# Optimization experiments

Measured on AMD Instinct MI355X. Metric: run time of the kernel, lower is better.

Reference implementation:

```python
import jax, jax.numpy as jnp
import numpy as np

BN_EPS = 1e-5
BIND_CHAN = 4  # hparams.MODEL.LEARNABLE_OFFSET.BIND_CHAN


def conv1x1(x, w, b):
    # x: [B,C,H,W], w: [O,C], b: [O]
    return jnp.einsum('bchw,oc->bohw', x, w) + b[None, :, None, None]


def bn_train(x, gamma, beta):
    # training-mode batch norm over (B,H,W) per channel
    mean = jnp.mean(x, axis=(0, 2, 3), keepdims=True)
    var = jnp.var(x, axis=(0, 2, 3), keepdims=True)
    xn = (x - mean) * jax.lax.rsqrt(var + BN_EPS)
    return xn * gamma[None, :, None, None] + beta[None, :, None, None]


def displace_channel(x, offsets):
    # x: [B,C,H,W]; offsets: [C,2] (dy,dx) per channel, continuous.
    # out[b,c,y,x] = bilinear sample of x[b,c] at (y+dy_c, x+dx_c), zeros outside.
    B, C, H, W = x.shape
    dy, dx = offsets[:, 0], offsets[:, 1]
    fy, fx = jnp.floor(dy), jnp.floor(dx)
    wy, wx = dy - fy, dx - fx          # fractional weights, [C]
    iy, ix = fy.astype(jnp.int32), fx.astype(jnp.int32)
    chan = jnp.arange(C)[:, None, None]

    def shifted(oy, ox):
        ys = jnp.arange(H)[None, :] + oy[:, None]   # [C,H]
        xs = jnp.arange(W)[None, :] + ox[:, None]   # [C,W]
        valid = ((ys >= 0) & (ys < H))[:, :, None] & ((xs >= 0) & (xs < W))[:, None, :]
        ysc = jnp.clip(ys, 0, H - 1)
        xsc = jnp.clip(xs, 0, W - 1)
        g = x[:, chan, ysc[:, :, None], xsc[:, None, :]]   # [B,C,H,W]
        return g * valid.astype(x.dtype)[None]

    w00 = ((1 - wy) * (1 - wx))[None, :, None, None]
    w01 = ((1 - wy) * wx)[None, :, None, None]
    w10 = (wy * (1 - wx))[None, :, None, None]
    w11 = (wy * wx)[None, :, None, None]
    return (w00 * shifted(iy, ix) + w01 * shifted(iy, ix + 1)
            + w10 * shifted(iy + 1, ix) + w11 * shifted(iy + 1, ix + 1))


def setup_inputs() -> dict:
    key = jax.random.key(0)
    ks = jax.random.split(key, 12)
    B, Cin, H, W = 16, 64, 128, 128
    Cd, Cout = 128, 64
    n_off = Cd // BIND_CHAN  # 32
    s_in = 1.0 / np.sqrt(Cin)
    s_d = 1.0 / np.sqrt(Cd)
    return {
        'x': jax.random.normal(ks[0], (B, Cin, H, W), jnp.float32),
        'pre_w': jax.random.uniform(ks[1], (Cd, Cin), jnp.float32, -s_in, s_in),
        'pre_b': jax.random.uniform(ks[2], (Cd,), jnp.float32, -s_in, s_in),
        'post_w': jax.random.uniform(ks[3], (Cout, Cd), jnp.float32, -s_d, s_d),
        'post_b': jax.random.uniform(ks[4], (Cout,), jnp.float32, -s_d, s_d),
        'atten_w': jax.random.uniform(ks[5], (Cd, Cin), jnp.float32, -s_in, s_in),
        'atten_b': jax.random.uniform(ks[6], (Cd,), jnp.float32, -s_in, s_in),
        'atten_bn_g': jnp.ones((Cd,), jnp.float32),
        'atten_bn_b': jnp.zeros((Cd,), jnp.float32),
        'offsets': jax.random.normal(ks[7], (n_off, 2), jnp.float32) * 3.0,
        'bn_g': jnp.ones((Cout,), jnp.float32),
        'bn_b': jnp.zeros((Cout,), jnp.float32),
    }


def reference(x, pre_w, pre_b, post_w, post_b, atten_w, atten_b,
              atten_bn_g, atten_bn_b, offsets, bn_g, bn_b):
    # pre_offset conv1x1
    out_pre = conv1x1(x, pre_w, pre_b)                        # [B,Cd,H,W]
    # DisplaceChannel: each offset shared by BIND_CHAN consecutive channels
    off_per_chan = jnp.repeat(offsets, BIND_CHAN, axis=0)     # [Cd,2]
    out_dis = displace_channel(out_pre, off_per_chan)
    # Attention branch: conv1x1 -> BN -> Softplus -> SpaceNormalization
    a = conv1x1(x, atten_w, atten_b)
    a = bn_train(a, atten_bn_g, atten_bn_b)
    a = jax.nn.softplus(a)
    out_atten = a / jnp.sum(a, axis=(2, 3), keepdims=True)    # spatial normalization
    # post_offset conv1x1 on gated displaced features
    out_post = conv1x1(out_atten * out_dis, post_w, post_b)
    # residual (inplanes == outplanes, stride 1 -> no downsample) + BN + ReLU
    out_skip = x + out_post
    return jax.nn.relu(bn_train(out_skip, bn_g, bn_b))
```

## Files before the change

### kernel.cpp

```cpp
#include <hip/hip_runtime.h>

#define HWSZ   16384
#define CIN    64
#define CD     128
#define COUT   64
#define BN_EPS 1e-5f

typedef __attribute__((ext_vector_type(8))) short short8x;
typedef __attribute__((ext_vector_type(4))) float floatx4;

#define WS_WT1   0
#define WS_WTP   16384
#define WS_DISP  24576
#define WS_ASTAT 25344
#define WS_OSTAT 25600
#define WS_BIG   32768
#define WS_TOTAL_BYTES ((size_t)(32768 + 16777216) * 4)

__device__ __forceinline__ unsigned short f2bf(float f) {
    unsigned int u = __float_as_uint(f);
    u += 0x7fff + ((u >> 16) & 1);
    return (unsigned short)(u >> 16);
}
__device__ __forceinline__ float bf2f(unsigned short s) {
    return __uint_as_float(((unsigned int)s) << 16);
}
__device__ __forceinline__ float softplus_fast(float x) {
    return fmaxf(x, 0.f) + __logf(1.f + __expf(-fabsf(x)));
}
__device__ __forceinline__ float block_reduce(float v, float* sc) {
    #pragma unroll
    for (int off = 32; off >= 1; off >>= 1) v += __shfl_xor(v, off, 64);
    int wv = threadIdx.x >> 6, ln = threadIdx.x & 63;
    int nw = blockDim.x >> 6;
    if (ln == 0) sc[wv] = v;
    __syncthreads();
    float r = ((int)threadIdx.x < nw) ? sc[threadIdx.x] : 0.f;
    r += __shfl_xor(r, 1, 64);
    r += __shfl_xor(r, 2, 64);
    r += __shfl_xor(r, 4, 64);
    return r;
}

__global__ __launch_bounds__(256) void prep_kernel(
        const float* __restrict__ pre_w, const float* __restrict__ atten_w,
        const float* __restrict__ post_w, const float* __restrict__ offsets,
        float* __restrict__ ws) {
    int tid = blockIdx.x * 256 + threadIdx.x;
    unsigned short* wAB = (unsigned short*)(ws + WS_WT1);
    unsigned short* wP  = (unsigned short*)(ws + WS_WTP);
    float* disp = ws + WS_DISP;
    if (tid < 16384) {
        int o = tid >> 6, c = tid & 63;
        float v = (o < 128) ? pre_w[o * 64 + c] : atten_w[(o - 128) * 64 + c];
        wAB[tid] = f2bf(v);
    } else if (tid < 24576) {
        int k = tid - 16384;
        int o = k >> 7, c = k & 127;
        wP[k] = f2bf(post_w[o * 128 + c]);
    } else if (tid < 24704) {
        int c = tid - 24576;
        float dy = offsets[(c >> 2) * 2 + 0];
        float dx = offsets[(c >> 2) * 2 + 1];
        float fy = floorf(dy), fx = floorf(dx);
        float wy = dy - fy, wx = dx - fx;
        float* d = disp + c * 6;
        d[0] = fy; d[1] = fx;
        d[2] = (1.f - wy) * (1.f - wx);
        d[3] = (1.f - wy) * wx;
        d[4] = wy * (1.f - wx);
        d[5] = wy * wx;
    }
}

__device__ __forceinline__ void pre_write_lds(unsigned short* wbuf, int c, int wv,
                                              const float4 ld[4]) {
    #pragma unroll
    for (int k = 0; k < 4; ++k) {
        int px = wv * 16 + k * 4;
        wbuf[(px + 0) * 72 + c] = f2bf(ld[k].x);
        wbuf[(px + 1) * 72 + c] = f2bf(ld[k].y);
        wbuf[(px + 2) * 72 + c] = f2bf(ld[k].z);
        wbuf[(px + 3) * 72 + c] = f2bf(ld[k].w);
    }
}

__device__ __forceinline__ void pre_compute_tile(
        const unsigned short* buf, int ln, int o0, int b, int ptile,
        const short8x wfrag[4][2], const float4 biasv[4],
        unsigned short* __restrict__ out_pre, unsigned short* __restrict__ a_out) {
    floatx4 acc[4][4];
    #pragma unroll
    for (int oi = 0; oi < 4; ++oi)
        #pragma unroll
        for (int pi = 0; pi < 4; ++pi)
            acc[oi][pi] = floatx4{biasv[oi].x, biasv[oi].y, biasv[oi].z, biasv[oi].w};
    #pragma unroll
    for (int kk = 0; kk < 2; ++kk)
        #pragma unroll
        for (int pi = 0; pi < 4; ++pi) {
            short8x xfrag = *(const short8x*)((const char*)buf +
                    (pi * 16 + (ln & 15)) * 144 + (kk * 32 + (ln >> 4) * 8) * 2);
            #pragma unroll
            for (int oi = 0; oi < 4; ++oi)
                acc[oi][pi] = __builtin_amdgcn_mfma_f32_16x16x32_bf16(
                        wfrag[oi][kk], xfrag, acc[oi][pi], 0, 0, 0);
        }
    #pragma unroll
    for (int oi = 0; oi < 4; ++oi) {
        int og = o0 + oi * 16;
        unsigned short* dst = (og < 128) ? out_pre : a_out;
        int ob = (og < 128) ? og : og - 128;
        #pragma unroll
        for (int pi = 0; pi < 4; ++pi) {
            int px = ptile + pi * 16 + (ln & 15);
            #pragma unroll
            for (int r = 0; r < 4; ++r) {
                int o = ob + (ln >> 4) * 4 + r;
                dst[((size_t)b * CD + o) * HWSZ + px] = f2bf(acc[oi][pi][r]);
            }
        }
    }
}

__global__ __launch_bounds__(256) void conv_pre_mfma(
        const float* __restrict__ x, const unsigned short* __restrict__ wAB,
        const float* __restrict__ pre_b, const float* __restrict__ atten_b,
        unsigned short* __restrict__ out_pre, unsigned short* __restrict__ a_out) {
    __shared__ unsigned short xT[2][64 * 72];
    int t = threadIdx.x;
    int wv = t >> 6, ln = t & 63;
    int b = blockIdx.x >> 6;
    int poff = (blockIdx.x & 63) << 8;
    const float* xg = x + (size_t)b * CIN * HWSZ + poff;
    int c = ln;

    int o0 = wv * 64;
    short8x wfrag[4][2];
    #pragma unroll
    for (int oi = 0; oi < 4; ++oi)
        #pragma unroll
        for (int kk = 0; kk < 2; ++kk) {
            int row = o0 + oi * 16 + (ln & 15);
            int kcol = kk * 32 + (ln >> 4) * 8;
            wfrag[oi][kk] = *(const short8x*)(wAB + row * 64 + kcol);
        }
    float4 biasv[4];
    #pragma unroll
    for (int oi = 0; oi < 4; ++oi) {
        int og = o0 + oi * 16;
        const float* bias = (og < 128) ? (pre_b + og) : (atten_b + og - 128);
        biasv[oi] = *(const float4*)(bias + (ln >> 4) * 4);
    }

    float4 lda[4], ldb[4];
    #pragma unroll
    for (int k = 0; k < 4; ++k)
        lda[k] = *(const float4*)(xg + (size_t)c * HWSZ + 0 * 64 + wv * 16 + k * 4);
    pre_write_lds(xT[0], c, wv, lda);
    #pragma unroll
    for (int k = 0; k < 4; ++k)
        lda[k] = *(const float4*)(xg + (size_t)c * HWSZ + 1 * 64 + wv * 16 + k * 4);
    __syncthreads();

    #pragma unroll
    for (int k = 0; k < 4; ++k)
        ldb[k] = *(const float4*)(xg + (size_t)c * HWSZ + 2 * 64 + wv * 16 + k * 4);
    pre_compute_tile(xT[0], ln, o0, b, poff + 0 * 64, wfrag, biasv, out_pre, a_out);
    pre_write_lds(xT[1], c, wv, lda);
    __syncthreads();

    #pragma unroll
    for (int k = 0; k < 4; ++k)
        lda[k] = *(const float4*)(xg + (size_t)c * HWSZ + 3 * 64 + wv * 16 + k * 4);
    pre_compute_tile(xT[1], ln, o0, b, poff + 1 * 64, wfrag, biasv, out_pre, a_out);
    pre_write_lds(xT[0], c, wv, ldb);
    __syncthreads();

    pre_compute_tile(xT[0], ln, o0, b, poff + 2 * 64, wfrag, biasv, out_pre, a_out);
    pre_write_lds(xT[1], c, wv, lda);
    __syncthreads();

    pre_compute_tile(xT[1], ln, o0, b, poff + 3 * 64, wfrag, biasv, out_pre, a_out);
}

__global__ __launch_bounds__(256) void chan_stats_bf16(
        const unsigned short* __restrict__ src, float* __restrict__ stats) {
    __shared__ float sc1[8], sc2[8];
    int c = blockIdx.x, b = blockIdx.y;
    const unsigned short* base = src + ((size_t)b * CD + c) * HWSZ;
    int t = threadIdx.x;
    float sum = 0.f, sq = 0.f;
    #pragma unroll
    for (int i = 0; i < 8; ++i) {
        uint4 v = *(const uint4*)(base + i * 2048 + t * 8);
        unsigned int u[4] = {v.x, v.y, v.z, v.w};
        #pragma unroll
        for (int k = 0; k < 4; ++k) {
            float lo = bf2f((unsigned short)(u[k] & 0xffff));
            float hi = bf2f((unsigned short)(u[k] >> 16));
            sum += lo + hi;
            sq  += lo * lo + hi * hi;
        }
    }
    sum = block_reduce(sum, sc1);
    __syncthreads();
    sq = block_reduce(sq, sc2);
    if (t == 0) {
        atomicAdd(&stats[c * 2 + 0], sum);
        atomicAdd(&stats[c * 2 + 1], sq);
    }
}

struct Win9 { float v0,v1,v2,v3,v4,v5,v6,v7,v8; };
__device__ __forceinline__ Win9 extract9(uint4 qa, uint4 qb, bool s4, int sh) {
    unsigned long long A0 = ((unsigned long long)qa.y << 32) | qa.x;
    unsigned long long A1 = ((unsigned long long)qa.w << 32) | qa.z;
    unsigned long long A2 = ((unsigned long long)qb.y << 32) | qb.x;
    unsigned long long A3 = ((unsigned long long)qb.w << 32) | qb.z;
    unsigned long long B0 = s4 ? A1 : A0;
    unsigned long long B1 = s4 ? A2 : A1;
    unsigned long long B2 = s4 ? A3 : A2;
    unsigned long long r0 = sh ? ((B0 >> sh) | (B1 << (64 - sh))) : B0;
    unsigned long long r1 = sh ? ((B1 >> sh) | (B2 << (64 - sh))) : B1;
    unsigned int v8w = (unsigned int)(sh ? (B2 >> sh) : B2);
    Win9 w;
    w.v0 = bf2f((unsigned short)(r0 >>  0)); w.v1 = bf2f((unsigned short)(r0 >> 16));
    w.v2 = bf2f((unsigned short)(r0 >> 32)); w.v3 = bf2f((unsigned short)(r0 >> 48));
    w.v4 = bf2f((unsigned short)(r1 >>  0)); w.v5 = bf2f((unsigned short)(r1 >> 16));
    w.v6 = bf2f((unsigned short)(r1 >> 32)); w.v7 = bf2f((unsigned short)(r1 >> 48));
    w.v8 = bf2f((unsigned short)(v8w & 0xffff));
    return w;
}

__global__ __launch_bounds__(512) void displace_bnsp_mul(
        unsigned short* __restrict__ pre, const unsigned short* __restrict__ a_raw,
        const float* __restrict__ stats, const float* __restrict__ g,
        const float* __restrict__ bb, const float* __restrict__ disp) {
    __shared__ unsigned short img[128 * 136];
    __shared__ float sc[8];
    __shared__ float s_inv;
    int bc = blockIdx.x;
    int cc = bc & 127;
    const float* d = disp + cc * 6;
    int iy = (int)d[0], ix = (int)d[1];
    float w00 = d[2], w01 = d[3], w10 = d[4], w11 = d[5];
    const float N = 262144.f;
    float mean = stats[cc * 2] / N;
    float var  = stats[cc * 2 + 1] / N - mean * mean;
    float rstd = rsqrtf(var + BN_EPS);
    float scl = rstd * g[cc];
    float shf = bb[cc] - mean * scl;
    unsigned short* pb = pre + (size_t)bc * HWSZ;
    const unsigned short* ab = a_raw + (size_t)bc * HWSZ;
    int t = threadIdx.x;
    uint4 aspr[4];
    float lsum = 0.f;
    #pragma unroll
    for (int i = 0; i < 4; ++i) {
        int px = i * 4096 + t * 8;
        uint4 v = *(const uint4*)(pb + px);
        int y = px >> 7, xx = px & 127;
        *(uint4*)&img[y * 136 + xx] = v;
        uint4 av = *(const uint4*)(ab + px);
        unsigned int au[4] = {av.x, av.y, av.z, av.w};
        unsigned int ou[4];
        #pragma unroll
        for (int k = 0; k < 4; ++k) {
            float lo = softplus_fast(bf2f((unsigned short)(au[k] & 0xffff)) * scl + shf);
            float hi = softplus_fast(bf2f((unsigned short)(au[k] >> 16))    * scl + shf);
            lsum += lo + hi;
            ou[k] = (unsigned int)f2bf(lo) | ((unsigned int)f2bf(hi) << 16);
        }
        aspr[i] = uint4{ou[0], ou[1], ou[2], ou[3]};
    }
    lsum = block_reduce(lsum, sc);
    if (t == 0) s_inv = 1.f / lsum;
    __syncthreads();
    float inv = s_inv;
    int s = ix & 7;
    int ix8 = ix - s;
    int sh = (s & 3) * 16;
    bool s4 = s >= 4;
    #pragma unroll
    for (int i = 0; i < 4; ++i) {
        int px = i * 4096 + t * 8;
        int y = px >> 7, x0 = px & 127;
        int yy0 = y + iy, yy1 = yy0 + 1;
        float wA0 = (yy0 >= 0 && yy0 < 128) ? w00 : 0.f;
        float wA1 = (yy0 >= 0 && yy0 < 128) ? w01 : 0.f;
        float wB0 = (yy1 >= 0 && yy1 < 128) ? w10 : 0.f;
        float wB1 = (yy1 >= 0 && yy1 < 128) ? w11 : 0.f;
        int yc0 = min(max(yy0, 0), 127), yc1 = min(max(yy1, 0), 127);
        int w0 = x0 + ix8;
        uint4 z = {0u, 0u, 0u, 0u};
        uint4 qa0 = (w0 >= 0 && w0 <= 120)         ? *(const uint4*)&img[yc0 * 136 + w0]     : z;
        uint4 qa1 = (w0 + 8 >= 0 && w0 + 8 <= 120) ? *(const uint4*)&img[yc0 * 136 + w0 + 8] : z;
        uint4 qb0 = (w0 >= 0 && w0 <= 120)         ? *(const uint4*)&img[yc1 * 136 + w0]     : z;
        uint4 qb1 = (w0 + 8 >= 0 && w0 + 8 <= 120) ? *(const uint4*)&img[yc1 * 136 + w0 + 8] : z;
        Win9 va = extract9(qa0, qa1, s4, sh);
        Win9 vb = extract9(qb0, qb1, s4, sh);
        float dv0 = wA0*va.v0 + wA1*va.v1 + wB0*vb.v0 + wB1*vb.v1;
        float dv1 = wA0*va.v1 + wA1*va.v2 + wB0*vb.v1 + wB1*vb.v2;
        float dv2 = wA0*va.v2 + wA1*va.v3 + wB0*vb.v2 + wB1*vb.v3;
        float dv3 = wA0*va.v3 + wA1*va.v4 + wB0*vb.v3 + wB1*vb.v4;
        float dv4 = wA0*va.v4 + wA1*va.v5 + wB0*vb.v4 + wB1*vb.v5;
        float dv5 = wA0*va.v5 + wA1*va.v6 + wB0*vb.v5 + wB1*vb.v6;
        float dv6 = wA0*va.v6 + wA1*va.v7 + wB0*vb.v6 + wB1*vb.v7;
        float dv7 = wA0*va.v7 + wA1*va.v8 + wB0*vb.v7 + wB1*vb.v8;
        unsigned int au[4] = {aspr[i].x, aspr[i].y, aspr[i].z, aspr[i].w};
        float a0 = bf2f((unsigned short)(au[0] & 0xffff)) * inv;
        float a1 = bf2f((unsigned short)(au[0] >> 16)) * inv;
        float a2 = bf2f((unsigned short)(au[1] & 0xffff)) * inv;
        float a3 = bf2f((unsigned short)(au[1] >> 16)) * inv;
        float a4 = bf2f((unsigned short)(au[2] & 0xffff)) * inv;
        float a5 = bf2f((unsigned short)(au[2] >> 16)) * inv;
        float a6 = bf2f((unsigned short)(au[3] & 0xffff)) * inv;
        float a7 = bf2f((unsigned short)(au[3] >> 16)) * inv;
        uint4 o;
        o.x = (unsigned int)f2bf(dv0 * a0) | ((unsigned int)f2bf(dv1 * a1) << 16);
        o.y = (unsigned int)f2bf(dv2 * a2) | ((unsigned int)f2bf(dv3 * a3) << 16);
        o.z = (unsigned int)f2bf(dv4 * a4) | ((unsigned int)f2bf(dv5 * a5) << 16);
        o.w = (unsigned int)f2bf(dv6 * a6) | ((unsigned int)f2bf(dv7 * a7) << 16);
        *(uint4*)(pb + px) = o;
    }
}

__global__ __launch_bounds__(256) void conv_post_mfma(
        const unsigned short* __restrict__ m, const unsigned short* __restrict__ wP,
        const float* __restrict__ post_b, const float* __restrict__ x,
        unsigned short* __restrict__ skipS) {
    __shared__ unsigned short mT[128 * 128];
    int t = threadIdx.x;
    int P0 = blockIdx.x * 128;
    int b = P0 >> 14, poff = P0 & 16383;
    int cl = t & 31, q = t >> 5;
    #pragma unroll
    for (int pass = 0; pass < 4; ++pass) {
        int c = cl + pass * 32;
        const unsigned short* mrow = m + ((size_t)b * CD + c) * HWSZ + poff;
        #pragma unroll
        for (int h = 0; h < 2; ++h) {
            int px0 = h * 64 + q * 8;
            uint4 v = *(const uint4*)(mrow + px0);
            unsigned int u[4] = {v.x, v.y, v.z, v.w};
            #pragma unroll
            for (int j = 0; j < 8; ++j) {
                unsigned short val = (unsigned short)((u[j >> 1] >> ((j & 1) * 16)) & 0xffff);
                int byteoff = (px0 + j) * 256 + ((c * 2) ^ (j << 4));
                *(unsigned short*)((char*)mT + byteoff) = val;
            }
        }
    }
    __syncthreads();
    int ln = t & 63, wv = t >> 6;
    int o0 = (wv >> 1) * 32;
    int ph = (wv & 1) * 64;
    short8x aw[2][4];
    #pragma unroll
    for (int oi = 0; oi < 2; ++oi)
        #pragma unroll
        for (int kk = 0; kk < 4; ++kk)
            aw[oi][kk] = *(const short8x*)(wP + (o0 + oi * 16 + (ln & 15)) * 128 + kk * 32 + (ln >> 4) * 8);
    floatx4 acc[2][4];
    #pragma unroll
    for (int oi = 0; oi < 2; ++oi)
        #pragma unroll
        for (int pi = 0; pi < 4; ++pi) acc[oi][pi] = floatx4{0.f, 0.f, 0.f, 0.f};
    #pragma unroll
    for (int kk = 0; kk < 4; ++kk)
        #pragma unroll
        for (int pi = 0; pi < 4; ++pi) {
            int px = ph + pi * 16 + (ln & 15);
            int cb = kk * 64 + (ln >> 4) * 16;
            short8x bf = *(const short8x*)((const char*)mT + px * 256 + (cb ^ ((px & 7) << 4)));
            #pragma unroll
            for (int oi = 0; oi < 2; ++oi)
                acc[oi][pi] = __builtin_amdgcn_mfma_f32_16x16x32_bf16(aw[oi][kk], bf, acc[oi][pi], 0, 0, 0);
        }
    #pragma unroll
    for (int oi = 0; oi < 2; ++oi) {
        float4 b4 = *(const float4*)(post_b + o0 + oi * 16 + (ln >> 4) * 4);
        float bb[4] = {b4.x, b4.y, b4.z, b4.w};
        #pragma unroll
        for (int pi = 0; pi < 4; ++pi) {
            int pxg = poff + ph + pi * 16 + (ln & 15);
            #pragma unroll
            for (int r = 0; r < 4; ++r) {
                int o = o0 + oi * 16 + (ln >> 4) * 4 + r;
                float val = acc[oi][pi][r] + bb[r] + x[((size_t)b * COUT + o) * HWSZ + pxg];
                skipS[((size_t)b * CD + o) * HWSZ + pxg] = f2bf(val);
            }
        }
    }
}

__global__ __launch_bounds__(256) void bn_relu_out(
        const unsigned short* __restrict__ skipS, float* __restrict__ out,
        const float* __restrict__ stats, const float* __restrict__ g,
        const float* __restrict__ bb) {
    const float N = 262144.f;
    int t = threadIdx.x;
    #pragma unroll
    for (int k = 0; k < 4; ++k) {
        size_t gidx = (size_t)blockIdx.x * 1024 + k * 256 + t;
        size_t e = gidx * 8;
        int b = (int)(e >> 20);
        int c = (int)(e >> 14) & 63;
        int px = (int)(e & 16383);
        float mean = stats[c * 2] / N;
        float rstd = rsqrtf(stats[c * 2 + 1] / N - mean * mean + BN_EPS);
        float gc = g[c], bbc = bb[c];
        uint4 v = *(const uint4*)(skipS + ((size_t)b * CD + c) * HWSZ + px);
        unsigned int u[4] = {v.x, v.y, v.z, v.w};
        float4 o0, o1;
        float* op[8] = {&o0.x, &o0.y, &o0.z, &o0.w, &o1.x, &o1.y, &o1.z, &o1.w};
        #pragma unroll
        for (int j = 0; j < 8; ++j) {
            float val = bf2f((unsigned short)((u[j >> 1] >> ((j & 1) * 16)) & 0xffff));
            *op[j] = fmaxf((val - mean) * rstd * gc + bbc, 0.f);
        }
        *(float4*)(out + e) = o0;
        *(float4*)(out + e + 4) = o1;
    }
}

extern "C" void kernel_launch(void* const* d_in, const int* in_sizes, int n_in,
                              void* d_out, int out_size, void* d_ws, size_t ws_size,
                              hipStream_t stream) {
    const float* x          = (const float*)d_in[0];
    const float* pre_w      = (const float*)d_in[1];
    const float* pre_b      = (const float*)d_in[2];
    const float* post_w     = (const float*)d_in[3];
    const float* post_b     = (const float*)d_in[4];
    const float* atten_w    = (const float*)d_in[5];
    const float* atten_b    = (const float*)d_in[6];
    const float* atten_bn_g = (const float*)d_in[7];
    const float* atten_bn_b = (const float*)d_in[8];
    const float* offsets    = (const float*)d_in[9];
    const float* bn_g       = (const float*)d_in[10];
    const float* bn_b       = (const float*)d_in[11];
    float* out = (float*)d_out;
    float* ws  = (float*)d_ws;

    if (ws_size < WS_TOTAL_BYTES) return;

    unsigned short* wAB = (unsigned short*)(ws + WS_WT1);
    unsigned short* wP  = (unsigned short*)(ws + WS_WTP);
    float* disp    = ws + WS_DISP;
    float* a_stats = ws + WS_ASTAT;
    float* o_stats = ws + WS_OSTAT;
    unsigned short* big   = (unsigned short*)(ws + WS_BIG);
    unsigned short* a_buf = (unsigned short*)d_out;

    hipMemsetAsync((void*)a_stats, 0, 384 * sizeof(float), stream);

    prep_kernel<<<97, 256, 0, stream>>>(pre_w, atten_w, post_w, offsets, ws);
    conv_pre_mfma<<<1024, 256, 0, stream>>>(x, wAB, pre_b, atten_b, big, a_buf);
    chan_stats_bf16<<<dim3(128, 16), 256, 0, stream>>>(a_buf, a_stats);
    displace_bnsp_mul<<<2048, 512, 0, stream>>>(big, a_buf, a_stats, atten_bn_g, atten_bn_b, disp);
    conv_post_mfma<<<2048, 256, 0, stream>>>(big, wP, post_b, x, big);
    chan_stats_bf16<<<dim3(64, 16), 256, 0, stream>>>(big, o_stats);
    bn_relu_out<<<2048, 256, 0, stream>>>(big, out, o_stats, bn_g, bn_b);
}
```

Measured before the change: 163.0 us.

## Drop prep kernel and read displace windows directly from global memory

Removes the separate prep kernel. Weight-to-bf16 conversion moves into the conv kernels' fragment loads, and the offset/bilinear weight computation moves into the displace kernel. The displace kernel no longer stages the whole channel image in LDS. It gathers the shifted windows straight from global memory (served by L1/L2) and writes the gated result in place over the attention buffer. The post conv then reads from that buffer. This saves one launch and frees a large LDS allocation for higher occupancy, at the cost of redundant global gathers and repeated weight conversion in every block.

```diff
diff --git a/kernel.cpp b/kernel.cpp
--- a/kernel.cpp
+++ b/kernel.cpp
@@ -9,9 +9,6 @@
 typedef __attribute__((ext_vector_type(8))) short short8x;
 typedef __attribute__((ext_vector_type(4))) float floatx4;
 
-#define WS_WT1   0
-#define WS_WTP   16384
-#define WS_DISP  24576
 #define WS_ASTAT 25344
 #define WS_OSTAT 25600
 #define WS_BIG   32768
@@ -42,35 +39,15 @@
     return r;
 }
 
-__global__ __launch_bounds__(256) void prep_kernel(
-        const float* __restrict__ pre_w, const float* __restrict__ atten_w,
-        const float* __restrict__ post_w, const float* __restrict__ offsets,
-        float* __restrict__ ws) {
-    int tid = blockIdx.x * 256 + threadIdx.x;
-    unsigned short* wAB = (unsigned short*)(ws + WS_WT1);
-    unsigned short* wP  = (unsigned short*)(ws + WS_WTP);
-    float* disp = ws + WS_DISP;
-    if (tid < 16384) {
-        int o = tid >> 6, c = tid & 63;
-        float v = (o < 128) ? pre_w[o * 64 + c] : atten_w[(o - 128) * 64 + c];
-        wAB[tid] = f2bf(v);
-    } else if (tid < 24576) {
-        int k = tid - 16384;
-        int o = k >> 7, c = k & 127;
-        wP[k] = f2bf(post_w[o * 128 + c]);
-    } else if (tid < 24704) {
-        int c = tid - 24576;
-        float dy = offsets[(c >> 2) * 2 + 0];
-        float dx = offsets[(c >> 2) * 2 + 1];
-        float fy = floorf(dy), fx = floorf(dx);
-        float wy = dy - fy, wx = dx - fx;
-        float* d = disp + c * 6;
-        d[0] = fy; d[1] = fx;
-        d[2] = (1.f - wy) * (1.f - wx);
-        d[3] = (1.f - wy) * wx;
-        d[4] = wy * (1.f - wx);
-        d[5] = wy * wx;
-    }
+__device__ __forceinline__ short8x cvt_w8(const float* src) {
+    float4 f0 = *(const float4*)(src);
+    float4 f1 = *(const float4*)(src + 4);
+    short8x w;
+    w[0] = (short)f2bf(f0.x); w[1] = (short)f2bf(f0.y);
+    w[2] = (short)f2bf(f0.z); w[3] = (short)f2bf(f0.w);
+    w[4] = (short)f2bf(f1.x); w[5] = (short)f2bf(f1.y);
+    w[6] = (short)f2bf(f1.z); w[7] = (short)f2bf(f1.w);
+    return w;
 }
 
 __device__ __forceinline__ void pre_write_lds(unsigned short* wbuf, int c, int wv,
@@ -124,7 +101,8 @@
 }
 
 __global__ __launch_bounds__(256) void conv_pre_mfma(
-        const float* __restrict__ x, const unsigned short* __restrict__ wAB,
+        const float* __restrict__ x, const float* __restrict__ pre_w,
+        const float* __restrict__ atten_w,
         const float* __restrict__ pre_b, const float* __restrict__ atten_b,
         unsigned short* __restrict__ out_pre, unsigned short* __restrict__ a_out) {
     __shared__ unsigned short xT[2][64 * 72];
@@ -143,7 +121,9 @@
         for (int kk = 0; kk < 2; ++kk) {
             int row = o0 + oi * 16 + (ln & 15);
             int kcol = kk * 32 + (ln >> 4) * 8;
-            wfrag[oi][kk] = *(const short8x*)(wAB + row * 64 + kcol);
+            const float* wsrc = (row < 128) ? (pre_w + row * 64)
+                                            : (atten_w + (row - 128) * 64);
+            wfrag[oi][kk] = cvt_w8(wsrc + kcol);
         }
     float4 biasv[4];
     #pragma unroll
@@ -233,36 +213,38 @@
     return w;
 }
 
-__global__ __launch_bounds__(512) void displace_bnsp_mul(
-        unsigned short* __restrict__ pre, const unsigned short* __restrict__ a_raw,
+__global__ __launch_bounds__(512) void displace_bnsp_gg(
+        const unsigned short* __restrict__ pre, unsigned short* __restrict__ a_m,
         const float* __restrict__ stats, const float* __restrict__ g,
-        const float* __restrict__ bb, const float* __restrict__ disp) {
-    __shared__ unsigned short img[128 * 136];
+        const float* __restrict__ bb, const float* __restrict__ offsets) {
     __shared__ float sc[8];
     __shared__ float s_inv;
     int bc = blockIdx.x;
     int cc = bc & 127;
-    const float* d = disp + cc * 6;
-    int iy = (int)d[0], ix = (int)d[1];
-    float w00 = d[2], w01 = d[3], w10 = d[4], w11 = d[5];
+    float dy = offsets[(cc >> 2) * 2 + 0];
+    float dx = offsets[(cc >> 2) * 2 + 1];
+    float fy = floorf(dy), fx = floorf(dx);
+    float wy = dy - fy, wx = dx - fx;
+    int iy = (int)fy, ix = (int)fx;
+    float w00 = (1.f - wy) * (1.f - wx);
+    float w01 = (1.f - wy) * wx;
+    float w10 = wy * (1.f - wx);
+    float w11 = wy * wx;
     const float N = 262144.f;
     float mean = stats[cc * 2] / N;
     float var  = stats[cc * 2 + 1] / N - mean * mean;
     float rstd = rsqrtf(var + BN_EPS);
     float scl = rstd * g[cc];
     float shf = bb[cc] - mean * scl;
-    unsigned short* pb = pre + (size_t)bc * HWSZ;
-    const unsigned short* ab = a_raw + (size_t)bc * HWSZ;
+    const unsigned short* pg = pre + (size_t)bc * HWSZ;
+    unsigned short* am = a_m + (size_t)bc * HWSZ;
     int t = threadIdx.x;
     uint4 aspr[4];
     float lsum = 0.f;
     #pragma unroll
     for (int i = 0; i < 4; ++i) {
         int px = i * 4096 + t * 8;
-        uint4 v = *(const uint4*)(pb + px);
-        int y = px >> 7, xx = px & 127;
-        *(uint4*)&img[y * 136 + xx] = v;
-        uint4 av = *(const uint4*)(ab + px);
+        uint4 av = *(const uint4*)(am + px);
         unsigned int au[4] = {av.x, av.y, av.z, av.w};
         unsigned int ou[4];
         #pragma unroll
@@ -294,10 +276,10 @@
         int yc0 = min(max(yy0, 0), 127), yc1 = min(max(yy1, 0), 127);
         int w0 = x0 + ix8;
         uint4 z = {0u, 0u, 0u, 0u};
-        uint4 qa0 = (w0 >= 0 && w0 <= 120)         ? *(const uint4*)&img[yc0 * 136 + w0]     : z;
-        uint4 qa1 = (w0 + 8 >= 0 && w0 + 8 <= 120) ? *(const uint4*)&img[yc0 * 136 + w0 + 8] : z;
-        uint4 qb0 = (w0 >= 0 && w0 <= 120)         ? *(const uint4*)&img[yc1 * 136 + w0]     : z;
-        uint4 qb1 = (w0 + 8 >= 0 && w0 + 8 <= 120) ? *(const uint4*)&img[yc1 * 136 + w0 + 8] : z;
+        uint4 qa0 = (w0 >= 0 && w0 <= 120)         ? *(const uint4*)(pg + yc0 * 128 + w0)     : z;
+        uint4 qa1 = (w0 + 8 >= 0 && w0 + 8 <= 120) ? *(const uint4*)(pg + yc0 * 128 + w0 + 8) : z;
+        uint4 qb0 = (w0 >= 0 && w0 <= 120)         ? *(const uint4*)(pg + yc1 * 128 + w0)     : z;
+        uint4 qb1 = (w0 + 8 >= 0 && w0 + 8 <= 120) ? *(const uint4*)(pg + yc1 * 128 + w0 + 8) : z;
         Win9 va = extract9(qa0, qa1, s4, sh);
         Win9 vb = extract9(qb0, qb1, s4, sh);
         float dv0 = wA0*va.v0 + wA1*va.v1 + wB0*vb.v0 + wB1*vb.v1;
@@ -322,12 +304,12 @@
         o.y = (unsigned int)f2bf(dv2 * a2) | ((unsigned int)f2bf(dv3 * a3) << 16);
         o.z = (unsigned int)f2bf(dv4 * a4) | ((unsigned int)f2bf(dv5 * a5) << 16);
         o.w = (unsigned int)f2bf(dv6 * a6) | ((unsigned int)f2bf(dv7 * a7) << 16);
-        *(uint4*)(pb + px) = o;
+        *(uint4*)(am + px) = o;
     }
 }
 
 __global__ __launch_bounds__(256) void conv_post_mfma(
-        const unsigned short* __restrict__ m, const unsigned short* __restrict__ wP,
+        const unsigned short* __restrict__ m, const float* __restrict__ post_w,
         const float* __restrict__ post_b, const float* __restrict__ x,
         unsigned short* __restrict__ skipS) {
     __shared__ unsigned short mT[128 * 128];
@@ -360,8 +342,10 @@
     #pragma unroll
     for (int oi = 0; oi < 2; ++oi)
         #pragma unroll
-        for (int kk = 0; kk < 4; ++kk)
-            aw[oi][kk] = *(const short8x*)(wP + (o0 + oi * 16 + (ln & 15)) * 128 + kk * 32 + (ln >> 4) * 8);
+        for (int kk = 0; kk < 4; ++kk) {
+            int o = o0 + oi * 16 + (ln & 15);
+            aw[oi][kk] = cvt_w8(post_w + o * 128 + kk * 32 + (ln >> 4) * 8);
+        }
     floatx4 acc[2][4];
     #pragma unroll
     for (int oi = 0; oi < 2; ++oi)
@@ -445,9 +429,6 @@
 
     if (ws_size < WS_TOTAL_BYTES) return;
 
-    unsigned short* wAB = (unsigned short*)(ws + WS_WT1);
-    unsigned short* wP  = (unsigned short*)(ws + WS_WTP);
-    float* disp    = ws + WS_DISP;
     float* a_stats = ws + WS_ASTAT;
     float* o_stats = ws + WS_OSTAT;
     unsigned short* big   = (unsigned short*)(ws + WS_BIG);
@@ -455,11 +436,10 @@
 
     hipMemsetAsync((void*)a_stats, 0, 384 * sizeof(float), stream);
 
-    prep_kernel<<<97, 256, 0, stream>>>(pre_w, atten_w, post_w, offsets, ws);
-    conv_pre_mfma<<<1024, 256, 0, stream>>>(x, wAB, pre_b, atten_b, big, a_buf);
+    conv_pre_mfma<<<1024, 256, 0, stream>>>(x, pre_w, atten_w, pre_b, atten_b, big, a_buf);
     chan_stats_bf16<<<dim3(128, 16), 256, 0, stream>>>(a_buf, a_stats);
-    displace_bnsp_mul<<<2048, 512, 0, stream>>>(big, a_buf, a_stats, atten_bn_g, atten_bn_b, disp);
-    conv_post_mfma<<<2048, 256, 0, stream>>>(big, wP, post_b, x, big);
+    displace_bnsp_gg<<<2048, 512, 0, stream>>>(big, a_buf, a_stats, atten_bn_g, atten_bn_b, offsets);
+    conv_post_mfma<<<2048, 256, 0, stream>>>(a_buf, post_w, post_b, x, big);
     chan_stats_bf16<<<dim3(64, 16), 256, 0, stream>>>(big, o_stats);
     bn_relu_out<<<2048, 256, 0, stream>>>(big, out, o_stats, bn_g, bn_b);
 }
```

After: 185.6 us. 1.14x slower.
